# Kernel tuning notes

Measured on AMD Instinct MI355X. Metric: run time of the kernel, lower is better.

## Reference

```python
import jax, jax.numpy as jnp
import numpy as np

N = 30000      # input points
M = 7500       # sampled queries = floor(N * ratio), ratio=0.25
K = 16         # neighbors per query
D_X = 64       # input feature dim
D_REL = 64     # point_pos_nn output dim
D_F = D_X + D_REL  # fij_hat dim = 128


def setup_inputs() -> dict:
    key = jax.random.key(0)
    ks = jax.random.split(key, 6)
    x = jax.random.normal(ks[0], (N, D_X), jnp.float32)
    pos = jax.random.normal(ks[1], (N, 3), jnp.float32)
    idx = jax.random.randint(ks[2], (M,), 0, N)
    W_pos = jax.random.normal(ks[3], (10, D_REL), jnp.float32) / jnp.sqrt(10.0)
    b_pos = jnp.zeros((D_REL,), jnp.float32)
    W_att = jax.random.normal(ks[4], (D_F, D_F), jnp.float32) / jnp.sqrt(float(D_F))
    b_att = jnp.zeros((D_F,), jnp.float32)
    W_glob = jax.random.normal(ks[5], (D_F, D_F), jnp.float32) / jnp.sqrt(float(D_F))
    b_glob = jnp.zeros((D_F,), jnp.float32)
    return {"x": x, "pos": pos, "idx": idx, "W_pos": W_pos, "b_pos": b_pos,
            "W_att": W_att, "b_att": b_att, "W_glob": W_glob, "b_glob": b_glob}


def reference(x, pos, idx, W_pos, b_pos, W_att, b_att, W_glob, b_glob):
    # --- KNN: brute-force squared distances from sampled queries to all points ---
    pos_q = pos[idx]                                         # [M, 3]
    d2 = ((pos_q * pos_q).sum(-1)[:, None]
          + (pos * pos).sum(-1)[None, :]
          - 2.0 * pos_q @ pos.T)                             # [M, N]
    _, nbr = jax.lax.top_k(-d2, K)                           # [M, K] neighbor indices

    # --- Local Spatial Encoding (message) ---
    pos_j = pos[nbr]                                         # [M, K, 3]
    pos_i = jnp.broadcast_to(pos_q[:, None, :], pos_j.shape) # [M, K, 3]
    vij = pos_i - pos_j                                      # [M, K, 3]
    dij = jnp.linalg.norm(vij, axis=-1, keepdims=True)       # [M, K, 1]
    rel = jnp.concatenate([pos_i, pos_j, vij, dij], axis=-1) # [M, K, 10]
    rij = jax.nn.relu(rel @ W_pos + b_pos)                   # [M, K, D_REL]

    # --- Attentive pooling ---
    fij = jnp.concatenate([x[nbr], rij], axis=-1)            # [M, K, D_F]
    g = fij @ W_att + b_att                                  # [M, K, D_F]
    s = jax.nn.softmax(g, axis=-1)                           # softmax over feature dim
    aggr = jnp.mean(s * fij, axis=1)                         # mean over K neighbors -> [M, D_F]

    # --- global_nn (update) ---
    return jax.nn.relu(aggr @ W_glob + b_glob)               # [M, D_F]
```

## Files before the change

kernel.cpp:

```cpp
#include <hip/hip_runtime.h>
#include <stdint.h>

#define KNB     16
#define GD      64
#define GTOT    (GD * GD * GD)
#define GORIG   (-6.5f)
#define GEDGE   0.203125f
#define GINV    (1.0f / GEDGE)
#define CAPW    640
#define PROBE_T 48

typedef short short8 __attribute__((ext_vector_type(8)));
typedef float floatx4 __attribute__((ext_vector_type(4)));

__device__ __forceinline__ unsigned short f2bf(float x) {
  union { float f; uint32_t u; } v; v.f = x;
  uint32_t u = v.u + 0x7FFFu + ((v.u >> 16) & 1u);
  return (unsigned short)(u >> 16);
}
__device__ __forceinline__ float bf2f(unsigned short b) {
  return __uint_as_float(((uint32_t)b) << 16);
}
__device__ __forceinline__ int cellco(float v) {
  int c = (int)floorf((v - GORIG) * GINV);
  return c < 0 ? 0 : (c > GD - 1 ? GD - 1 : c);
}

__global__ void zero_kernel(int* __restrict__ count) {
  int i = (blockIdx.x * 256 + threadIdx.x) * 4;
  *(int4*)(count + i) = make_int4(0, 0, 0, 0);
}

__global__ void prep_kernel(const float* __restrict__ x,
                            const float* __restrict__ pos,
                            const float* __restrict__ W_att,
                            unsigned short* __restrict__ xb,
                            float4* __restrict__ pos4,
                            unsigned short* __restrict__ Wt,
                            int* __restrict__ ptcell,
                            int* __restrict__ count, int N) {
  int id = blockIdx.x * 256 + threadIdx.x;
  int nx8 = N * 8;
  if (id < nx8) {
    const float4* src = (const float4*)x + (size_t)id * 2;
    float4 a = src[0], b = src[1];
    short8 v;
    v[0] = (short)f2bf(a.x); v[1] = (short)f2bf(a.y);
    v[2] = (short)f2bf(a.z); v[3] = (short)f2bf(a.w);
    v[4] = (short)f2bf(b.x); v[5] = (short)f2bf(b.y);
    v[6] = (short)f2bf(b.z); v[7] = (short)f2bf(b.w);
    *(short8*)(xb + (size_t)id * 8) = v;
  } else if (id < nx8 + N) {
    int j = id - nx8;
    float px = pos[3 * j], py = pos[3 * j + 1], pz = pos[3 * j + 2];
    float pp = fmaf(px, px, fmaf(py, py, pz * pz));
    pos4[j] = make_float4(px, py, pz, pp);
    int cid = (cellco(pz) * GD + cellco(py)) * GD + cellco(px);
    ptcell[j] = cid;
    atomicAdd(&count[cid], 1);
  } else if (id < nx8 + N + 128 * 128) {
    int t = id - nx8 - N;
    int c = t >> 7, f = t & 127;
    Wt[f * 128 + c] = f2bf(W_att[t]);
  }
}

__global__ __launch_bounds__(256) void vscan_x(const int* __restrict__ count,
                                               int* __restrict__ V) {
  int row = blockIdx.x * 4 + (threadIdx.x >> 6);
  int ln = threadIdx.x & 63;
  int i = row * GD + ln;
  int v = count[i];
#pragma unroll
  for (int off = 1; off < 64; off <<= 1) {
    int y = __shfl_up(v, off);
    if (ln >= off) v += y;
  }
  V[i] = v;
}

__global__ __launch_bounds__(256) void vscan_y(int* __restrict__ V) {
  int pair = blockIdx.x * 4 + (threadIdx.x >> 6);
  int z = pair >> 6, x = pair & 63;
  int ln = threadIdx.x & 63;
  int i = (z * GD + ln) * GD + x;
  int v = V[i];
#pragma unroll
  for (int off = 1; off < 64; off <<= 1) {
    int y = __shfl_up(v, off);
    if (ln >= off) v += y;
  }
  V[i] = v;
}

__global__ __launch_bounds__(256) void vscan_z(int* __restrict__ V) {
  int pair = blockIdx.x * 4 + (threadIdx.x >> 6);
  int ln = threadIdx.x & 63;
  int i = ln * GD * GD + pair;
  int v = V[i];
#pragma unroll
  for (int off = 1; off < 64; off <<= 1) {
    int y = __shfl_up(v, off);
    if (ln >= off) v += y;
  }
  V[i] = v;
}

__global__ __launch_bounds__(256) void derive_kernel(
    const int* __restrict__ V, int* __restrict__ cell_start,
    int* __restrict__ cursor) {
  int cid = blockIdx.x * 256 + threadIdx.x;
  int x = cid & 63, y = (cid >> 6) & 63, z = cid >> 12;
  int s = 0;
  if (z > 0) s += V[((z - 1) * GD + 63) * GD + 63];
  if (y > 0) {
    s += V[(z * GD + (y - 1)) * GD + 63];
    if (z > 0) s -= V[((z - 1) * GD + (y - 1)) * GD + 63];
  }
  if (x > 0) {
    s += V[(z * GD + y) * GD + (x - 1)];
    if (y > 0) s -= V[(z * GD + (y - 1)) * GD + (x - 1)];
    if (z > 0) s -= V[((z - 1) * GD + y) * GD + (x - 1)];
    if (z > 0 && y > 0) s += V[((z - 1) * GD + (y - 1)) * GD + (x - 1)];
  }
  cell_start[cid] = s;
  cursor[cid] = s;
  if (cid == 0) cell_start[GTOT] = V[GTOT - 1];
}

__global__ void scatter_kernel(const float4* __restrict__ pos4,
                               const int* __restrict__ ptcell,
                               int* __restrict__ cursor,
                               float4* __restrict__ spos4, int N) {
  int j = blockIdx.x * 256 + threadIdx.x;
  if (j >= N) return;
  int cid = ptcell[j];
  int slot = atomicAdd(&cursor[cid], 1);
  float4 p = pos4[j];
  spos4[slot] = make_float4(p.x, p.y, p.z, __int_as_float(j));
}

__device__ __forceinline__ unsigned long long top16_reg(
    unsigned long long* candw, int tot, int ln) {
  unsigned long long c[CAPW / 64];
#pragma unroll
  for (int chk = 0; chk < CAPW / 64; ++chk) {
    int slot = chk * 64 + ln;
    c[chk] = (slot < tot) ? candw[slot] : ~0ull;
  }
  unsigned long long mykey = ~0ull, last = 0;
#pragma unroll
  for (int r = 0; r < KNB; ++r) {
    unsigned long long mn = c[0];
#pragma unroll
    for (int chk = 1; chk < CAPW / 64; ++chk) mn = (c[chk] < mn) ? c[chk] : mn;
#pragma unroll
    for (int off = 1; off < 64; off <<= 1) {
      unsigned long long o = __shfl_xor(mn, off);
      mn = (o < mn) ? o : mn;
    }
    if (ln == r) mykey = mn;
    last = mn;
#pragma unroll
    for (int chk = 0; chk < CAPW / 64; ++chk)
      if (c[chk] == mn) c[chk] = ~0ull;
  }
  if (ln < KNB) candw[ln] = mykey;
  return last;
}

__device__ __forceinline__ void drain_annulus(
    const float4* __restrict__ spos4, const int* __restrict__ cell_start,
    unsigned long long* candw, float4 qp, int cqx, int cqy, int cqz,
    int slo, int shi, int ln, int& tot, unsigned long long& taukey) {
  const int z0 = (cqz - shi < 0) ? 0 : cqz - shi;
  const int z1 = (cqz + shi > GD - 1) ? GD - 1 : cqz + shi;
  const int y0 = (cqy - shi < 0) ? 0 : cqy - shi;
  const int y1 = (cqy + shi > GD - 1) ? GD - 1 : cqy + shi;
  const int wy = y1 - y0 + 1;
  const int npair = (z1 - z0 + 1) * wy;
  for (int base = 0; base < npair; base += 64) {
    int i = base + ln;
    int stA = 0, lA = 0, stB = 0, lB = 0;
    if (i < npair) {
      int zz = z0 + i / wy;
      int yy = y0 + (i - (i / wy) * wy);
      int dz = zz - cqz, dy = yy - cqy;
      int az = dz < 0 ? -dz : dz, ay = dy < 0 ? -dy : dy;
      int ch = az > ay ? az : ay;
      int rowbase = (zz * GD + yy) * GD;
      if (ch > slo) {
        int x0 = cqx - shi; if (x0 < 0) x0 = 0;
        int x1 = cqx + shi; if (x1 > GD - 1) x1 = GD - 1;
        stA = cell_start[rowbase + x0];
        lA  = cell_start[rowbase + x1 + 1] - stA;
      } else {
        int xl0 = cqx - shi; if (xl0 < 0) xl0 = 0;
        int xl1 = cqx - slo - 1;
        if (xl1 >= xl0) {
          stA = cell_start[rowbase + xl0];
          lA  = cell_start[rowbase + xl1 + 1] - stA;
        }
        int xr0 = cqx + slo + 1;
        int xr1 = cqx + shi; if (xr1 > GD - 1) xr1 = GD - 1;
        if (xr1 >= xr0) {
          stB = cell_start[rowbase + xr0];
          lB  = cell_start[rowbase + xr1 + 1] - stB;
        }
      }
    }
    int len = lA + lB;
    int xinc = len;
#pragma unroll
    for (int off = 1; off < 64; off <<= 1) {
      int y = __shfl_up(xinc, off);
      if (ln >= off) xinc += y;
    }
    int T = __shfl(xinc, 63);
    if (T == 0) continue;
    int ps_ex = xinc - len;

    for (int b2 = 0; b2 < T; b2 += 128) {
      if (tot + 128 > CAPW) {
        taukey = top16_reg(candw, tot, ln);
        tot = KNB;
      }
      int flatA = b2 + ln;
      int flatB = b2 + 64 + ln;
      bool vA = flatA < T, vB = flatB < T;
      int fA = vA ? flatA : (T - 1);
      int fB = vB ? flatB : (T - 1);
      int loA = 0, loB = 0;
#pragma unroll
      for (int step = 32; step > 0; step >>= 1) {
        int mA = loA + step, mB = loB + step;
        int sA = __shfl(ps_ex, mA & 63);
        int sB = __shfl(ps_ex, mB & 63);
        if (mA <= 63 && sA <= fA) loA = mA;
        if (mB <= 63 && sB <= fB) loB = mB;
      }
      int psA = __shfl(ps_ex, loA), psB = __shfl(ps_ex, loB);
      int saA = __shfl(stA, loA),   saB = __shfl(stA, loB);
      int laA = __shfl(lA, loA),    laB = __shfl(lA, loB);
      int sbA = __shfl(stB, loA),   sbB = __shfl(stB, loB);
      int oA = fA - psA, oB = fB - psB;
      int pA = (oA < laA) ? (saA + oA) : (sbA + (oA - laA));
      int pB = (oB < laB) ? (saB + oB) : (sbB + (oB - laB));
      float4 pjA = spos4[pA];
      float4 pjB = spos4[pB];
      float ppA = fmaf(pjA.x, pjA.x, fmaf(pjA.y, pjA.y, pjA.z * pjA.z));
      float ppB = fmaf(pjB.x, pjB.x, fmaf(pjB.y, pjB.y, pjB.z * pjB.z));
      float dotA = fmaf(qp.x, pjA.x, fmaf(qp.y, pjA.y, qp.z * pjA.z));
      float dotB = fmaf(qp.x, pjB.x, fmaf(qp.y, pjB.y, qp.z * pjB.z));
      float d2A = fmaxf(qp.w + fmaf(-2.f, dotA, ppA), 0.f);
      float d2B = fmaxf(qp.w + fmaf(-2.f, dotB, ppB), 0.f);
      unsigned long long keyA =
          ((unsigned long long)__float_as_uint(d2A) << 32) |
          (uint32_t)__float_as_uint(pjA.w);
      unsigned long long keyB =
          ((unsigned long long)__float_as_uint(d2B) << 32) |
          (uint32_t)__float_as_uint(pjB.w);
      bool okA = vA && (keyA < taukey);
      bool okB = vB && (keyB < taukey);
      unsigned long long bmA = __ballot(okA);
      int posA = __popcll(bmA & ((1ull << ln) - 1ull));
      if (okA) candw[tot + posA] = keyA;
      tot += __popcll(bmA);
      unsigned long long bmB = __ballot(okB);
      int posB = __popcll(bmB & ((1ull << ln) - 1ull));
      if (okB) candw[tot + posB] = keyB;
      tot += __popcll(bmB);
    }
  }
}

__global__ __launch_bounds__(64) void knn_grid(
    const float4* __restrict__ pos4, const float4* __restrict__ spos4,
    const int* __restrict__ cell_start, const int* __restrict__ V,
    const int* __restrict__ idx, int* __restrict__ nbr, int M) {
  __shared__ unsigned long long cand[CAPW];
  const int ln = threadIdx.x;
  const int m = blockIdx.x;

  const float4 qp = pos4[idx[m]];
  const int cqx = cellco(qp.x), cqy = cellco(qp.y), cqz = cellco(qp.z);

  int s0;
  {
    int s = ln;
    int xh = cqx + s > GD - 1 ? GD - 1 : cqx + s;
    int yh = cqy + s > GD - 1 ? GD - 1 : cqy + s;
    int zh = cqz + s > GD - 1 ? GD - 1 : cqz + s;
    int xm = cqx - s - 1, ym = cqy - s - 1, zm = cqz - s - 1;
    int c = V[(zh * GD + yh) * GD + xh];
    if (zm >= 0) c -= V[(zm * GD + yh) * GD + xh];
    if (ym >= 0) c -= V[(zh * GD + ym) * GD + xh];
    if (xm >= 0) c -= V[(zh * GD + yh) * GD + xm];
    if (zm >= 0 && ym >= 0) c += V[(zm * GD + ym) * GD + xh];
    if (zm >= 0 && xm >= 0) c += V[(zm * GD + yh) * GD + xm];
    if (ym >= 0 && xm >= 0) c += V[(zh * GD + ym) * GD + xm];
    if (zm >= 0 && ym >= 0 && xm >= 0) c -= V[(zm * GD + ym) * GD + xm];
    unsigned long long bm = __ballot(c >= PROBE_T);
    s0 = __ffsll((unsigned long long)bm) - 1;
  }

  int tot = 0;
  unsigned long long taukey = ~0ull;
  drain_annulus(spos4, cell_start, cand, qp, cqx, cqy, cqz,
                -1, s0, ln, tot, taukey);
  taukey = top16_reg(cand, tot, ln);
  tot = KNB;
  float d16sq = __uint_as_float((uint32_t)(taukey >> 32));

  int s1 = s0;
  {
    float fx = qp.x - GORIG, fy = qp.y - GORIG, fz = qp.z - GORIG;
    while (s1 < GD - 1) {
      float r = 3.0e38f;
      if (cqx - s1 > 0)      r = fminf(r, fx - (float)(cqx - s1) * GEDGE);
      if (cqx + s1 < GD - 1) r = fminf(r, (float)(cqx + s1 + 1) * GEDGE - fx);
      if (cqy - s1 > 0)      r = fminf(r, fy - (float)(cqy - s1) * GEDGE);
      if (cqy + s1 < GD - 1) r = fminf(r, (float)(cqy + s1 + 1) * GEDGE - fy);
      if (cqz - s1 > 0)      r = fminf(r, fz - (float)(cqz - s1) * GEDGE);
      if (cqz + s1 < GD - 1) r = fminf(r, (float)(cqz + s1 + 1) * GEDGE - fz);
      float r2 = (r > 1.0e19f) ? 3.0e38f : r * r;
      if (r2 >= d16sq) break;
      ++s1;
    }
  }

  if (s1 > s0) {
    drain_annulus(spos4, cell_start, cand, qp, cqx, cqy, cqz,
                  s0, s1, ln, tot, taukey);
    if (tot > KNB) (void)top16_reg(cand, tot, ln);
  }

  if (ln < KNB) nbr[m * KNB + ln] = (int)(uint32_t)cand[ln];
}

__global__ __launch_bounds__(256) void mid_kernel(
    const unsigned short* __restrict__ xb, const float4* __restrict__ pos4,
    const int* __restrict__ idx, const float* __restrict__ W_pos,
    const float* __restrict__ b_pos, const unsigned short* __restrict__ Wt,
    const float* __restrict__ b_att, const int* __restrict__ nbr,
    float* __restrict__ aggr, int M) {
  __shared__ __align__(16) unsigned short fijb[8][16][136];
  __shared__ int nbr_s[128];
  __shared__ float4 qpos_s[8];

  const int tid = threadIdx.x;
  const int wid = tid >> 6, lane = tid & 63;
  const int col = lane & 15, quad = lane >> 4;
  const int b = blockIdx.x;

  if (tid < 128) {
    int mq = b * 8 + (tid >> 4); if (mq >= M) mq = M - 1;
    nbr_s[tid] = nbr[mq * 16 + (tid & 15)];
  }
  if (tid < 8) {
    int mq = b * 8 + tid; if (mq >= M) mq = M - 1;
    qpos_s[tid] = pos4[idx[mq]];
  }
  float wp[10];
#pragma unroll
  for (int t = 0; t < 10; ++t) wp[t] = W_pos[t * 64 + lane];
  float bp = b_pos[lane];
  __syncthreads();

  {
    int rr = tid >> 1, h = tid & 1;
    int jn = nbr_s[rr];
    const short8* src = (const short8*)(xb + ((size_t)jn << 6) + (h << 5));
    short8 v0 = src[0], v1 = src[1], v2 = src[2], v3 = src[3];
    short8* dst = (short8*)&fijb[rr >> 4][rr & 15][h * 32];
    dst[0] = v0; dst[1] = v1; dst[2] = v2; dst[3] = v3;
  }
#pragma unroll
  for (int qi = 0; qi < 2; ++qi) {
    int q = wid * 2 + qi;
    float4 qp = qpos_s[q];
#pragma unroll 4
    for (int k = 0; k < 16; ++k) {
      int jn = nbr_s[q * 16 + k];
      float4 pj = pos4[jn];
      float vx = qp.x - pj.x, vy = qp.y - pj.y, vz = qp.z - pj.z;
      float dd = sqrtf(fmaf(vx, vx, fmaf(vy, vy, vz * vz)));
      float r = bp;
      r = fmaf(qp.x, wp[0], r); r = fmaf(qp.y, wp[1], r); r = fmaf(qp.z, wp[2], r);
      r = fmaf(pj.x, wp[3], r); r = fmaf(pj.y, wp[4], r); r = fmaf(pj.z, wp[5], r);
      r = fmaf(vx, wp[6], r);  r = fmaf(vy, wp[7], r);  r = fmaf(vz, wp[8], r);
      r = fmaf(dd, wp[9], r);
      r = fmaxf(r, 0.f);
      fijb[q][k][64 + lane] = f2bf(r);
    }
  }
  __syncthreads();

#pragma unroll 1
  for (int qi = 0; qi < 2; ++qi) {
    int q = wid * 2 + qi;
    int mq = b * 8 + q;

    short8 af[4];
#pragma unroll
    for (int cs = 0; cs < 4; ++cs)
      af[cs] = *(const short8*)&fijb[q][col][cs * 32 + quad * 8];

    floatx4 acc[8];
#pragma unroll
    for (int ft = 0; ft < 8; ++ft) {
      float bav = b_att[ft * 16 + col];
      floatx4 a = {bav, bav, bav, bav};
#pragma unroll
      for (int cs = 0; cs < 4; ++cs) {
        short8 bfrag =
            *(const short8*)&Wt[(ft * 16 + col) * 128 + cs * 32 + quad * 8];
        a = __builtin_amdgcn_mfma_f32_16x16x32_bf16(af[cs], bfrag, a, 0, 0, 0);
      }
      acc[ft] = a;
    }

    float rowmax[4], rowinv[4];
#pragma unroll
    for (int r = 0; r < 4; ++r) {
      float mx = acc[0][r];
#pragma unroll
      for (int ft = 1; ft < 8; ++ft) mx = fmaxf(mx, acc[ft][r]);
      mx = fmaxf(mx, __shfl_xor(mx, 1));
      mx = fmaxf(mx, __shfl_xor(mx, 2));
      mx = fmaxf(mx, __shfl_xor(mx, 4));
      mx = fmaxf(mx, __shfl_xor(mx, 8));
      float sm = 0.f;
#pragma unroll
      for (int ft = 0; ft < 8; ++ft) sm += __expf(acc[ft][r] - mx);
      sm += __shfl_xor(sm, 1);
      sm += __shfl_xor(sm, 2);
      sm += __shfl_xor(sm, 4);
      sm += __shfl_xor(sm, 8);
      rowmax[r] = mx;
      rowinv[r] = 1.0f / sm;
    }

#pragma unroll
    for (int ft = 0; ft < 8; ++ft) {
      float ap = 0.f;
#pragma unroll
      for (int r = 0; r < 4; ++r) {
        float s = __expf(acc[ft][r] - rowmax[r]) * rowinv[r];
        float fv = bf2f(fijb[q][quad * 4 + r][ft * 16 + col]);
        ap = fmaf(s, fv, ap);
      }
      ap += __shfl_xor(ap, 16);
      ap += __shfl_xor(ap, 32);
      if (quad == 0 && mq < M)
        aggr[mq * 128 + ft * 16 + col] = ap * (1.0f / 16.0f);
    }
  }
}

__global__ __launch_bounds__(256) void out_kernel(
    const float* __restrict__ aggr, const float* __restrict__ W_glob,
    const float* __restrict__ b_glob, float* __restrict__ out, int M) {
  __shared__ float ag[16][128];
  const int tid = threadIdx.x;
  const int mbase = blockIdx.x * 16;
  for (int s = tid; s < 16 * 128; s += 256) {
    int r = s >> 7, cc = s & 127;
    int m = mbase + r;
    ((float*)ag)[s] = (m < M) ? aggr[m * 128 + cc] : 0.0f;
  }
  __syncthreads();
  const int f = tid & 127, h = tid >> 7;
  float acc[8];
  float bg = b_glob[f];
#pragma unroll
  for (int i = 0; i < 8; ++i) acc[i] = bg;
  for (int c = 0; c < 128; c += 4) {
    float w0 = W_glob[(c + 0) * 128 + f];
    float w1 = W_glob[(c + 1) * 128 + f];
    float w2 = W_glob[(c + 2) * 128 + f];
    float w3 = W_glob[(c + 3) * 128 + f];
#pragma unroll
    for (int i = 0; i < 8; ++i) {
      const floatx4 a4 = *(const floatx4*)&ag[h * 8 + i][c];
      acc[i] += a4[0] * w0 + a4[1] * w1 + a4[2] * w2 + a4[3] * w3;
    }
  }
#pragma unroll
  for (int i = 0; i < 8; ++i) {
    int m = mbase + h * 8 + i;
    if (m < M) out[m * 128 + f] = fmaxf(acc[i], 0.0f);
  }
}

extern "C" void kernel_launch(void* const* d_in, const int* in_sizes, int n_in,
                              void* d_out, int out_size, void* d_ws,
                              size_t ws_size, hipStream_t stream) {
  const float* x      = (const float*)d_in[0];
  const float* pos    = (const float*)d_in[1];
  const int*   idx    = (const int*)d_in[2];
  const float* W_pos  = (const float*)d_in[3];
  const float* b_pos  = (const float*)d_in[4];
  const float* W_att  = (const float*)d_in[5];
  const float* b_att  = (const float*)d_in[6];
  const float* W_glob = (const float*)d_in[7];
  const float* b_glob = (const float*)d_in[8];
  float* out = (float*)d_out;

  const int N = in_sizes[1] / 3;
  const int M = in_sizes[2];

  char* ws = (char*)d_ws;
  size_t o = 0;
  float4* pos4 = (float4*)(ws + o);               o += ((size_t)N * 16 + 255) & ~(size_t)255;
  unsigned short* xb = (unsigned short*)(ws + o); o += ((size_t)N * 128 + 255) & ~(size_t)255;
  unsigned short* Wt = (unsigned short*)(ws + o); o += (128 * 128 * 2 + 255) & ~(size_t)255;
  int* nbr = (int*)(ws + o);                      o += (((size_t)M * KNB * 4) + 255) & ~(size_t)255;
  int* ptcell = (int*)(ws + o);                   o += (((size_t)N * 4) + 255) & ~(size_t)255;
  int* count = (int*)(ws + o);                    o += ((size_t)GTOT * 4 + 255) & ~(size_t)255;
  int* cursor = (int*)(ws + o);                   o += ((size_t)GTOT * 4 + 255) & ~(size_t)255;
  int* cell_start = (int*)(ws + o);               o += ((size_t)(GTOT + 1) * 4 + 255) & ~(size_t)255;
  int* V = (int*)(ws + o);                        o += ((size_t)GTOT * 4 + 255) & ~(size_t)255;
  float4* spos4 = (float4*)(ws + o);              o += ((size_t)N * 16 + 255) & ~(size_t)255;
  float* aggr = (float*)(ws + o);                 o += ((size_t)M * 128 * 4 + 255) & ~(size_t)255;

  zero_kernel<<<GTOT / 1024, 256, 0, stream>>>(count);

  int prep_ids = N * 8 + N + 128 * 128;
  prep_kernel<<<(prep_ids + 255) / 256, 256, 0, stream>>>(
      x, pos, W_att, xb, pos4, Wt, ptcell, count, N);

  vscan_x<<<1024, 256, 0, stream>>>(count, V);
  vscan_y<<<1024, 256, 0, stream>>>(V);
  vscan_z<<<1024, 256, 0, stream>>>(V);
  derive_kernel<<<GTOT / 256, 256, 0, stream>>>(V, cell_start, cursor);

  scatter_kernel<<<(N + 255) / 256, 256, 0, stream>>>(pos4, ptcell, cursor,
                                                      spos4, N);

  knn_grid<<<M, 64, 0, stream>>>(pos4, spos4, cell_start, V, idx, nbr, M);

  mid_kernel<<<(M + 7) / 8, 256, 0, stream>>>(xb, pos4, idx, W_pos, b_pos, Wt,
                                              b_att, nbr, aggr, M);
  out_kernel<<<(M + 15) / 16, 256, 0, stream>>>(aggr, W_glob, b_glob, out, M);
}
```

Baseline: 203.0 us.

## Fuse global MLP into mid kernel, merge x/y grid scans, memset counts

```diff
diff --git a/kernel.cpp b/kernel.cpp
--- a/kernel.cpp
+++ b/kernel.cpp
@@ -24,11 +24,6 @@
 __device__ __forceinline__ int cellco(float v) {
   int c = (int)floorf((v - GORIG) * GINV);
   return c < 0 ? 0 : (c > GD - 1 ? GD - 1 : c);
-}
-
-__global__ void zero_kernel(int* __restrict__ count) {
-  int i = (blockIdx.x * 256 + threadIdx.x) * 4;
-  *(int4*)(count + i) = make_int4(0, 0, 0, 0);
 }
 
 __global__ void prep_kernel(const float* __restrict__ x,
@@ -65,32 +60,30 @@
   }
 }
 
-__global__ __launch_bounds__(256) void vscan_x(const int* __restrict__ count,
-                                               int* __restrict__ V) {
-  int row = blockIdx.x * 4 + (threadIdx.x >> 6);
-  int ln = threadIdx.x & 63;
-  int i = row * GD + ln;
-  int v = count[i];
-#pragma unroll
-  for (int off = 1; off < 64; off <<= 1) {
-    int y = __shfl_up(v, off);
-    if (ln >= off) v += y;
-  }
-  V[i] = v;
-}
-
-__global__ __launch_bounds__(256) void vscan_y(int* __restrict__ V) {
-  int pair = blockIdx.x * 4 + (threadIdx.x >> 6);
-  int z = pair >> 6, x = pair & 63;
-  int ln = threadIdx.x & 63;
-  int i = (z * GD + ln) * GD + x;
-  int v = V[i];
-#pragma unroll
-  for (int off = 1; off < 64; off <<= 1) {
-    int y = __shfl_up(v, off);
-    if (ln >= off) v += y;
-  }
-  V[i] = v;
+__global__ __launch_bounds__(256) void vscan_xy(const int* __restrict__ count,
+                                                int* __restrict__ V) {
+  __shared__ int slab[64][65];
+  const int z = blockIdx.x;
+  const int wv = threadIdx.x >> 6, ln = threadIdx.x & 63;
+  for (int r = wv; r < 64; r += 4) {
+    int v = count[(z * GD + r) * GD + ln];
+#pragma unroll
+    for (int off = 1; off < 64; off <<= 1) {
+      int y = __shfl_up(v, off);
+      if (ln >= off) v += y;
+    }
+    slab[r][ln] = v;
+  }
+  __syncthreads();
+  for (int c = wv; c < 64; c += 4) {
+    int v = slab[ln][c];
+#pragma unroll
+    for (int off = 1; off < 64; off <<= 1) {
+      int y = __shfl_up(v, off);
+      if (ln >= off) v += y;
+    }
+    V[(z * GD + ln) * GD + c] = v;
+  }
 }
 
 __global__ __launch_bounds__(256) void vscan_z(int* __restrict__ V) {
@@ -343,8 +336,10 @@
     const int* __restrict__ idx, const float* __restrict__ W_pos,
     const float* __restrict__ b_pos, const unsigned short* __restrict__ Wt,
     const float* __restrict__ b_att, const int* __restrict__ nbr,
-    float* __restrict__ aggr, int M) {
+    const float* __restrict__ W_glob, const float* __restrict__ b_glob,
+    float* __restrict__ out, int M) {
   __shared__ __align__(16) unsigned short fijb[8][16][136];
+  __shared__ float ag[8][128];
   __shared__ int nbr_s[128];
   __shared__ float4 qpos_s[8];
 
@@ -399,7 +394,6 @@
 #pragma unroll 1
   for (int qi = 0; qi < 2; ++qi) {
     int q = wid * 2 + qi;
-    int mq = b * 8 + q;
 
     short8 af[4];
 #pragma unroll
@@ -452,44 +446,34 @@
       }
       ap += __shfl_xor(ap, 16);
       ap += __shfl_xor(ap, 32);
-      if (quad == 0 && mq < M)
-        aggr[mq * 128 + ft * 16 + col] = ap * (1.0f / 16.0f);
-    }
-  }
-}
-
-__global__ __launch_bounds__(256) void out_kernel(
-    const float* __restrict__ aggr, const float* __restrict__ W_glob,
-    const float* __restrict__ b_glob, float* __restrict__ out, int M) {
-  __shared__ float ag[16][128];
-  const int tid = threadIdx.x;
-  const int mbase = blockIdx.x * 16;
-  for (int s = tid; s < 16 * 128; s += 256) {
-    int r = s >> 7, cc = s & 127;
-    int m = mbase + r;
-    ((float*)ag)[s] = (m < M) ? aggr[m * 128 + cc] : 0.0f;
+      if (quad == 0)
+        ag[q][ft * 16 + col] = ap * (1.0f / 16.0f);
+    }
   }
   __syncthreads();
-  const int f = tid & 127, h = tid >> 7;
-  float acc[8];
-  float bg = b_glob[f];
-#pragma unroll
-  for (int i = 0; i < 8; ++i) acc[i] = bg;
-  for (int c = 0; c < 128; c += 4) {
-    float w0 = W_glob[(c + 0) * 128 + f];
-    float w1 = W_glob[(c + 1) * 128 + f];
-    float w2 = W_glob[(c + 2) * 128 + f];
-    float w3 = W_glob[(c + 3) * 128 + f];
-#pragma unroll
-    for (int i = 0; i < 8; ++i) {
-      const floatx4 a4 = *(const floatx4*)&ag[h * 8 + i][c];
-      acc[i] += a4[0] * w0 + a4[1] * w1 + a4[2] * w2 + a4[3] * w3;
-    }
-  }
-#pragma unroll
-  for (int i = 0; i < 8; ++i) {
-    int m = mbase + h * 8 + i;
-    if (m < M) out[m * 128 + f] = fmaxf(acc[i], 0.0f);
+
+  {
+    const int f = tid & 127, h2 = tid >> 7;
+    float acc[4];
+    float bg = b_glob[f];
+#pragma unroll
+    for (int i = 0; i < 4; ++i) acc[i] = bg;
+    for (int c = 0; c < 128; c += 4) {
+      float w0 = W_glob[(c + 0) * 128 + f];
+      float w1 = W_glob[(c + 1) * 128 + f];
+      float w2 = W_glob[(c + 2) * 128 + f];
+      float w3 = W_glob[(c + 3) * 128 + f];
+#pragma unroll
+      for (int i = 0; i < 4; ++i) {
+        const floatx4 a4 = *(const floatx4*)&ag[h2 * 4 + i][c];
+        acc[i] += a4[0] * w0 + a4[1] * w1 + a4[2] * w2 + a4[3] * w3;
+      }
+    }
+#pragma unroll
+    for (int i = 0; i < 4; ++i) {
+      int m = b * 8 + h2 * 4 + i;
+      if (m < M) out[m * 128 + f] = fmaxf(acc[i], 0.0f);
+    }
   }
 }
 
@@ -522,16 +506,14 @@
   int* cell_start = (int*)(ws + o);               o += ((size_t)(GTOT + 1) * 4 + 255) & ~(size_t)255;
   int* V = (int*)(ws + o);                        o += ((size_t)GTOT * 4 + 255) & ~(size_t)255;
   float4* spos4 = (float4*)(ws + o);              o += ((size_t)N * 16 + 255) & ~(size_t)255;
-  float* aggr = (float*)(ws + o);                 o += ((size_t)M * 128 * 4 + 255) & ~(size_t)255;
-
-  zero_kernel<<<GTOT / 1024, 256, 0, stream>>>(count);
+
+  hipMemsetAsync(count, 0, (size_t)GTOT * 4, stream);
 
   int prep_ids = N * 8 + N + 128 * 128;
   prep_kernel<<<(prep_ids + 255) / 256, 256, 0, stream>>>(
       x, pos, W_att, xb, pos4, Wt, ptcell, count, N);
 
-  vscan_x<<<1024, 256, 0, stream>>>(count, V);
-  vscan_y<<<1024, 256, 0, stream>>>(V);
+  vscan_xy<<<GD, 256, 0, stream>>>(count, V);
   vscan_z<<<1024, 256, 0, stream>>>(V);
   derive_kernel<<<GTOT / 256, 256, 0, stream>>>(V, cell_start, cursor);
 
@@ -541,6 +523,6 @@
   knn_grid<<<M, 64, 0, stream>>>(pos4, spos4, cell_start, V, idx, nbr, M);
 
   mid_kernel<<<(M + 7) / 8, 256, 0, stream>>>(xb, pos4, idx, W_pos, b_pos, Wt,
-                                              b_att, nbr, aggr, M);
-  out_kernel<<<(M + 15) / 16, 256, 0, stream>>>(aggr, W_glob, b_glob, out, M);
-}
+                                              b_att, nbr, W_glob, b_glob, out,
+                                              M);
+}
```

Result: slower. 231.1 us (+13.8%).
